# Optimization experiments

Measured on AMD Instinct MI355X. Metric: run time of the kernel, lower is better.

## Reference

```python
import jax, jax.numpy as jnp
import numpy as np

N_HEADS = 8
WINDOW = 4

def setup_inputs() -> dict:
    key = jax.random.key(0)
    ks = jax.random.split(key, 12)
    B, C, L = 8, 512, 1024
    Dh = C // N_HEADS
    s = 1.0 / np.sqrt(C)
    inp = {
        'x': jax.random.normal(ks[0], (B, C, L), dtype=jnp.float32),
        'Wq': jax.random.normal(ks[1], (C, C), dtype=jnp.float32) * s,
        'bq': jnp.zeros((C,), dtype=jnp.float32),
        'Wk': jax.random.normal(ks[2], (C, C), dtype=jnp.float32) * s,
        'bk': jnp.zeros((C,), dtype=jnp.float32),
        'Wv': jax.random.normal(ks[3], (C, C), dtype=jnp.float32) * s,
        'bv': jnp.zeros((C,), dtype=jnp.float32),
        'Wo': jax.random.normal(ks[4], (C, C), dtype=jnp.float32) * s,
        'bo': jnp.zeros((C,), dtype=jnp.float32),
        'emb_rel_k': jax.random.normal(ks[5], (2 * WINDOW + 1, Dh), dtype=jnp.float32) * 0.02,
        'emb_rel_v': jax.random.normal(ks[6], (2 * WINDOW + 1, Dh), dtype=jnp.float32) * 0.02,
    }
    return inp


def reference(x, Wq, bq, Wk, bk, Wv, bv, Wo, bo, emb_rel_k, emb_rel_v):
    B, C, L = x.shape
    H = N_HEADS
    Dh = C // H
    scale = Dh ** -0.5

    def proj(W, b):
        # pointwise conv1d == channel-mixing matmul; (B,C,L) -> (B,H,L,Dh)
        y = jnp.einsum('oc,bcl->bol', W, x) + b[:, None]
        return y.reshape(B, H, Dh, L).transpose(0, 1, 3, 2)

    q = proj(Wq, bq) * scale
    k = proj(Wk, bk)
    v = proj(Wv, bv)

    scores = jnp.einsum('bhld,bhjd->bhlj', q, k)  # (B,H,L,L)

    t = jnp.arange(L)
    diff = t[None, :] - t[:, None]                      # (L,L)
    window_mask = (jnp.abs(diff) <= WINDOW)
    indices = jnp.clip(diff, -WINDOW, WINDOW) + WINDOW  # (L,L) in [0, 2w]

    rel_k = emb_rel_k[indices]                          # (L,L,Dh)
    rel_scores = jnp.einsum('bhld,ljd->bhlj', q, rel_k)
    scores = scores + rel_scores * window_mask[None, None, :, :]

    attn = jax.nn.softmax(scores, axis=-1)

    out = jnp.einsum('bhlj,bhjd->bhld', attn, v)
    rel_v = emb_rel_v[indices] * window_mask[:, :, None]  # (L,L,Dh)
    out = out + jnp.einsum('bhlj,ljd->bhld', attn, rel_v)

    out = out.transpose(0, 1, 3, 2).reshape(B, C, L)
    out = jnp.einsum('oc,bcl->bol', Wo, out) + bo[:, None]
    return out
```

## Files before the change

kernel.cpp:

```cpp
#include <hip/hip_runtime.h>
#include <math.h>

#define B_  8
#define H_  8
#define C_  512
#define L_  1024
#define DH  64
#define WIN 4

typedef __attribute__((ext_vector_type(8))) short short8;
typedef __attribute__((ext_vector_type(4))) float floatx4;

__device__ __forceinline__ unsigned short f2bf(float f) {
    unsigned int u = __float_as_uint(f);
    u = u + 0x7FFFu + ((u >> 16) & 1u);
    return (unsigned short)(u >> 16);
}
__device__ __forceinline__ float bf2f(unsigned short h) {
    return __uint_as_float(((unsigned int)h) << 16);
}
__device__ __forceinline__ unsigned short f2h(float f) {
    _Float16 h = (_Float16)f;
    return *reinterpret_cast<unsigned short*>(&h);
}

__global__ __launch_bounds__(256) void prep_kernel(
    const float* __restrict__ Wq, const float* __restrict__ Wk,
    const float* __restrict__ Wv, const float* __restrict__ Wo,
    const float* __restrict__ bq, const float* __restrict__ bk,
    const float* __restrict__ bv,
    unsigned short* __restrict__ Wqkv_hi,
    unsigned short* __restrict__ Wo_h,
    float* __restrict__ bqkv)
{
    const int i = blockIdx.x * 256 + threadIdx.x;
    float4 v; ushort4 h;

    v = ((const float4*)Wq)[i];
    h.x = f2bf(v.x); h.y = f2bf(v.y); h.z = f2bf(v.z); h.w = f2bf(v.w);
    ((ushort4*)Wqkv_hi)[i] = h;

    v = ((const float4*)Wk)[i];
    h.x = f2bf(v.x); h.y = f2bf(v.y); h.z = f2bf(v.z); h.w = f2bf(v.w);
    ((ushort4*)Wqkv_hi)[65536 + i] = h;

    v = ((const float4*)Wv)[i];
    h.x = f2bf(v.x); h.y = f2bf(v.y); h.z = f2bf(v.z); h.w = f2bf(v.w);
    ((ushort4*)Wqkv_hi)[131072 + i] = h;

    v = ((const float4*)Wo)[i];
    h.x = f2h(v.x); h.y = f2h(v.y); h.z = f2h(v.z); h.w = f2h(v.w);
    ((ushort4*)Wo_h)[i] = h;

    if (i < 512)       bqkv[i] = bq[i];
    else if (i < 1024) bqkv[i] = bk[i - 512];
    else if (i < 1536) bqkv[i] = bv[i - 1024];
}

__global__ __launch_bounds__(256) void transpose_kernel(
    const float* __restrict__ x, unsigned short* __restrict__ xT)
{
    __shared__ float tile[32][33];
    const int b  = blockIdx.z;
    const int cb = blockIdx.y * 32;
    const int lb = blockIdx.x * 32;
    const int t  = threadIdx.x;
    {
        const int l = t & 31, c0 = t >> 5;
#pragma unroll
        for (int p = 0; p < 4; ++p) {
            const int c = c0 + 8 * p;
            tile[c][l] = x[((size_t)b * C_ + cb + c) * L_ + lb + l];
        }
    }
    __syncthreads();
    {
        const int c = t & 31, l0 = t >> 5;
#pragma unroll
        for (int p = 0; p < 4; ++p) {
            const int l = l0 + 8 * p;
            xT[((size_t)b * L_ + lb + l) * C_ + cb + c] = f2bf(tile[c][l]);
        }
    }
}

__global__ __launch_bounds__(256) void qkv_gemm_kernel(
    const unsigned short* __restrict__ Wh, const float* __restrict__ bqkv,
    const unsigned short* __restrict__ xT,
    unsigned short* __restrict__ Qb, unsigned short* __restrict__ Kb,
    unsigned short* __restrict__ Vc)
{
    __shared__ __align__(16) unsigned short As[128][40];
    __shared__ __align__(16) unsigned short Bs[128][40];
    __shared__ __align__(16) unsigned short sT[128][66];

    const int b   = blockIdx.z;
    const int oB  = blockIdx.y * 128;
    const int mat = oB >> 9;
    const int ob  = oB & 511;
    const int lb  = blockIdx.x * 128;
    const int t  = threadIdx.x;
    const int w = t >> 6, lane = t & 63, quad = lane >> 4, lc = lane & 15;
    const int wm = w >> 1, wn = w & 1;

    const unsigned short* Wm = Wh + (size_t)mat * C_ * C_;

    floatx4 acc[4][4];
#pragma unroll
    for (int i = 0; i < 4; ++i)
#pragma unroll
        for (int j = 0; j < 4; ++j) acc[i][j] = (floatx4)0.f;

    const int c8 = (t & 3) * 8, r0 = t >> 2;
    for (int c0 = 0; c0 < C_; c0 += 32) {
#pragma unroll
        for (int p = 0; p < 2; ++p) {
            *reinterpret_cast<uint4*>(&As[r0 + 64 * p][c8]) =
                *reinterpret_cast<const uint4*>(&Wm[(size_t)(ob + r0 + 64 * p) * C_ + c0 + c8]);
            *reinterpret_cast<uint4*>(&Bs[r0 + 64 * p][c8]) =
                *reinterpret_cast<const uint4*>(&xT[((size_t)b * L_ + lb + r0 + 64 * p) * C_ + c0 + c8]);
        }
        __syncthreads();

        short8 a[4], bb[4];
#pragma unroll
        for (int mt = 0; mt < 4; ++mt)
            a[mt] = *reinterpret_cast<const short8*>(&As[wm * 64 + mt * 16 + lc][quad * 8]);
#pragma unroll
        for (int nt = 0; nt < 4; ++nt)
            bb[nt] = *reinterpret_cast<const short8*>(&Bs[wn * 64 + nt * 16 + lc][quad * 8]);
#pragma unroll
        for (int mt = 0; mt < 4; ++mt)
#pragma unroll
            for (int nt = 0; nt < 4; ++nt)
                acc[mt][nt] = __builtin_amdgcn_mfma_f32_16x16x32_bf16(a[mt], bb[nt], acc[mt][nt], 0, 0, 0);
        __syncthreads();
    }

    if (mat == 2) {
#pragma unroll
        for (int mt = 0; mt < 4; ++mt) {
#pragma unroll
            for (int r = 0; r < 4; ++r) {
                const int o  = ob + wm * 64 + mt * 16 + quad * 4 + r;
                const float bi = bqkv[1024 + o];
#pragma unroll
                for (int nt = 0; nt < 4; ++nt) {
                    const int l = lb + wn * 64 + nt * 16 + lc;
                    Vc[((size_t)b * C_ + o) * L_ + l] = f2bf(acc[mt][nt][r] + bi);
                }
            }
        }
    } else {
        const float scale = (mat == 0) ? 0.125f : 1.0f;
        unsigned short* dst = (mat == 0) ? Qb : Kb;
#pragma unroll
        for (int hh = 0; hh < 2; ++hh) {
            if (wm == hh) {
#pragma unroll
                for (int mt = 0; mt < 4; ++mt) {
#pragma unroll
                    for (int r = 0; r < 4; ++r) {
                        const int o  = ob + hh * 64 + mt * 16 + quad * 4 + r;
                        const float bi = bqkv[mat * 512 + o];
                        const int d  = mt * 16 + quad * 4 + r;
#pragma unroll
                        for (int nt = 0; nt < 4; ++nt) {
                            const int l = wn * 64 + nt * 16 + lc;
                            sT[l][d] = f2bf((acc[mt][nt][r] + bi) * scale);
                        }
                    }
                }
            }
            __syncthreads();
            {
                const int l  = t >> 1, hf = t & 1;
                const int h  = (ob >> 6) + hh;
                const size_t o = (((size_t)b * H_ + h) * L_ + lb + l) * DH + hf * 32;
                uint4 v0 = *reinterpret_cast<const uint4*>(&sT[l][hf * 32]);
                uint4 v1 = *reinterpret_cast<const uint4*>(&sT[l][hf * 32 + 8]);
                uint4 v2 = *reinterpret_cast<const uint4*>(&sT[l][hf * 32 + 16]);
                uint4 v3 = *reinterpret_cast<const uint4*>(&sT[l][hf * 32 + 24]);
                *reinterpret_cast<uint4*>(&dst[o])      = v0;
                *reinterpret_cast<uint4*>(&dst[o + 8])  = v1;
                *reinterpret_cast<uint4*>(&dst[o + 16]) = v2;
                *reinterpret_cast<uint4*>(&dst[o + 24]) = v3;
            }
            __syncthreads();
        }
    }
}

__global__ __launch_bounds__(512, 4) void attn_kernel8(
    const unsigned short* __restrict__ Qb,
    const unsigned short* __restrict__ Kb,
    const unsigned short* __restrict__ Vc,
    const float* __restrict__ erel_k, const float* __restrict__ erel_v,
    unsigned short* __restrict__ AOh)
{
    __shared__ __align__(16) unsigned short kst[2][64][68];
    __shared__ __align__(16) unsigned short vst[2][64][68];
    __shared__ __align__(16) unsigned short Pl[8][16][68];
    __shared__ float rs[128][9];
    __shared__ float rv[128][9];

    const int t  = threadIdx.x;
    const int bh = blockIdx.x;
    const int rt = blockIdx.y;
    const int b = bh >> 3, h = bh & 7;
    const int w = t >> 6, lane = t & 63, quad = lane >> 4, lc = lane & 15;
    const int row0 = rt * 128;
    const int rowW = row0 + w * 16;

    const size_t qkBase = (size_t)bh * L_ * DH;
    const size_t vBase  = ((size_t)b * C_ + h * DH) * L_;

    for (int i = lane; i < 16 * 9; i += 64) rv[w * 16 + i / 9][i % 9] = 0.f;

    short8 af[2];
#pragma unroll
    for (int kk = 0; kk < 2; ++kk)
        af[kk] = *reinterpret_cast<const short8*>(
            &Qb[qkBase + (size_t)(rowW + lc) * DH + kk * 32 + quad * 8]);

    {
        floatx4 rsa = (floatx4)0.f;
        const int drow = (lc < 9) ? lc : 8;
#pragma unroll
        for (int kk = 0; kk < 2; ++kk) {
            short8 bfr;
#pragma unroll
            for (int i = 0; i < 8; ++i)
                bfr[i] = (short)f2bf(erel_k[drow * 64 + kk * 32 + quad * 8 + i]);
            rsa = __builtin_amdgcn_mfma_f32_16x16x32_bf16(af[kk], bfr, rsa, 0, 0, 0);
        }
        if (lc < 9) {
#pragma unroll
            for (int r = 0; r < 4; ++r)
                rs[w * 16 + quad * 4 + r][lc] = rsa[r];
        }
    }

    const int jr = t >> 3, jc = (t & 7) * 8;
    *reinterpret_cast<uint4*>(&kst[0][jr][jc]) =
        *reinterpret_cast<const uint4*>(&Kb[qkBase + (size_t)jr * DH + jc]);
    *reinterpret_cast<uint4*>(&vst[0][jr][jc]) =
        *reinterpret_cast<const uint4*>(&Vc[vBase + (size_t)jr * L_ + jc]);
    __syncthreads();

    short8 ones;
#pragma unroll
    for (int j = 0; j < 8; ++j) ones[j] = (short)0x3F80;

    floatx4 acc_o[4], acc_l = (floatx4)0.f;
#pragma unroll
    for (int nt = 0; nt < 4; ++nt) acc_o[nt] = (floatx4)0.f;

    for (int jt = 0; jt < L_ / 64; ++jt) {
        const int j0  = jt * 64;
        const int cur = jt & 1;

        uint4 pk, pv;
        if (jt < L_ / 64 - 1) {
            const int j0n = j0 + 64;
            pk = *reinterpret_cast<const uint4*>(
                &Kb[qkBase + (size_t)(j0n + jr) * DH + jc]);
            pv = *reinterpret_cast<const uint4*>(
                &Vc[vBase + (size_t)jr * L_ + j0n + jc]);
        }

        floatx4 sacc[4];
#pragma unroll
        for (int nt = 0; nt < 4; ++nt) sacc[nt] = (floatx4)0.f;
#pragma unroll
        for (int nt = 0; nt < 4; ++nt)
#pragma unroll
            for (int kk = 0; kk < 2; ++kk) {
                const short8 kf = *reinterpret_cast<const short8*>(
                    &kst[cur][nt * 16 + lc][kk * 32 + quad * 8]);
                sacc[nt] = __builtin_amdgcn_mfma_f32_16x16x32_bf16(af[kk], kf, sacc[nt], 0, 0, 0);
            }

        const bool nearD = (j0 <= rowW + 15 + WIN) && (j0 + 63 >= rowW - WIN);
        if (nearD) {
#pragma unroll
            for (int nt = 0; nt < 4; ++nt) {
                const int jg = j0 + nt * 16 + lc;
#pragma unroll
                for (int r = 0; r < 4; ++r) {
                    const int diff = jg - (rowW + quad * 4 + r);
                    if (diff >= -WIN && diff <= WIN)
                        sacc[nt][r] += rs[w * 16 + quad * 4 + r][diff + WIN];
                }
            }
        }

#pragma unroll
        for (int nt = 0; nt < 4; ++nt)
#pragma unroll
            for (int r = 0; r < 4; ++r)
                Pl[w][quad * 4 + r][nt * 16 + lc] = f2bf(__expf(sacc[nt][r]));

        if (nearD) {
            for (int idx = lane; idx < 16 * 9; idx += 64) {
                const int r16 = idx / 9, dr = idx % 9;
                const int jg = rowW + r16 + dr - WIN;
                if (jg >= j0 && jg < j0 + 64 && jg >= 0 && jg < L_)
                    rv[w * 16 + r16][dr] += bf2f(Pl[w][r16][jg - j0]);
            }
        }

        short8 pf[2];
#pragma unroll
        for (int kk = 0; kk < 2; ++kk)
            pf[kk] = *reinterpret_cast<const short8*>(&Pl[w][lc][kk * 32 + quad * 8]);

#pragma unroll
        for (int kk = 0; kk < 2; ++kk)
            acc_l = __builtin_amdgcn_mfma_f32_16x16x32_bf16(pf[kk], ones, acc_l, 0, 0, 0);

#pragma unroll
        for (int nt = 0; nt < 4; ++nt)
#pragma unroll
            for (int kk = 0; kk < 2; ++kk) {
                const short8 vf = *reinterpret_cast<const short8*>(
                    &vst[cur][nt * 16 + lc][kk * 32 + quad * 8]);
                acc_o[nt] = __builtin_amdgcn_mfma_f32_16x16x32_bf16(pf[kk], vf, acc_o[nt], 0, 0, 0);
            }

        if (jt < L_ / 64 - 1) {
            *reinterpret_cast<uint4*>(&kst[1 - cur][jr][jc]) = pk;
            *reinterpret_cast<uint4*>(&vst[1 - cur][jr][jc]) = pv;
        }
        __syncthreads();
    }

#pragma unroll
    for (int nt = 0; nt < 4; ++nt) {
        const int d = nt * 16 + lc;
        float ev[9];
#pragma unroll
        for (int dr = 0; dr < 9; ++dr) ev[dr] = erel_v[dr * 64 + d];
#pragma unroll
        for (int r = 0; r < 4; ++r) {
            const int rloc = w * 16 + quad * 4 + r;
            float v = acc_o[nt][r];
#pragma unroll
            for (int dr = 0; dr < 9; ++dr) v += rv[rloc][dr] * ev[dr];
            Pl[w][quad * 4 + r][nt * 16 + lc] = f2h(v / acc_l[r]);
        }
    }
    {
        const int row = lane >> 2, ds8 = (lane & 3) * 16;
        const uint4 q0 = *reinterpret_cast<const uint4*>(&Pl[w][row][ds8]);
        const uint4 q1 = *reinterpret_cast<const uint4*>(&Pl[w][row][ds8 + 8]);
        const size_t o = ((size_t)b * L_ + rowW + row) * C_ + h * 64 + ds8;
        *reinterpret_cast<uint4*>(&AOh[o])     = q0;
        *reinterpret_cast<uint4*>(&AOh[o + 8]) = q1;
    }
}

__global__ __launch_bounds__(256) void out_gemm_kernel(
    const unsigned short* __restrict__ Wh,
    const float* __restrict__ bo,
    const unsigned short* __restrict__ Ah,
    float* __restrict__ Y)
{
    __shared__ __align__(16) unsigned short As_h[128][40];
    __shared__ __align__(16) unsigned short Bs_h[64][40];

    const int b  = blockIdx.z;
    const int ob = blockIdx.y * 128;
    const int lb = blockIdx.x * 64;
    const int t  = threadIdx.x;
    const int w = t >> 6, lane = t & 63, quad = lane >> 4, lc = lane & 15;
    const int wm = w >> 1, wn = w & 1;

    floatx4 acc[4][2];
#pragma unroll
    for (int i = 0; i < 4; ++i)
#pragma unroll
        for (int j = 0; j < 2; ++j) acc[i][j] = (floatx4)0.f;

    const int c8 = (t & 3) * 8, r0 = t >> 2;
    for (int c0 = 0; c0 < C_; c0 += 32) {
#pragma unroll
        for (int p = 0; p < 2; ++p)
            *reinterpret_cast<uint4*>(&As_h[r0 + 64 * p][c8]) =
                *reinterpret_cast<const uint4*>(&Wh[(size_t)(ob + r0 + 64 * p) * C_ + c0 + c8]);
        {
            const size_t g = ((size_t)b * L_ + lb + r0) * C_ + c0 + c8;
            *reinterpret_cast<uint4*>(&Bs_h[r0][c8]) =
                *reinterpret_cast<const uint4*>(&Ah[g]);
        }
        __syncthreads();

        short8 ah[4], bhf[2];
#pragma unroll
        for (int mt = 0; mt < 4; ++mt)
            ah[mt] = *reinterpret_cast<const short8*>(&As_h[wm * 64 + mt * 16 + lc][quad * 8]);
#pragma unroll
        for (int nt = 0; nt < 2; ++nt)
            bhf[nt] = *reinterpret_cast<const short8*>(&Bs_h[wn * 32 + nt * 16 + lc][quad * 8]);
#pragma unroll
        for (int mt = 0; mt < 4; ++mt)
#pragma unroll
            for (int nt = 0; nt < 2; ++nt)
                acc[mt][nt] = __builtin_amdgcn_mfma_f32_16x16x32_f16(ah[mt], bhf[nt], acc[mt][nt], 0, 0, 0);
        __syncthreads();
    }

#pragma unroll
    for (int mt = 0; mt < 4; ++mt) {
#pragma unroll
        for (int r = 0; r < 4; ++r) {
            const int o = ob + wm * 64 + mt * 16 + quad * 4 + r;
            const float bi = bo[o];
#pragma unroll
            for (int nt = 0; nt < 2; ++nt) {
                const int l = lb + wn * 32 + nt * 16 + lc;
                Y[((size_t)b * C_ + o) * L_ + l] = acc[mt][nt][r] + bi;
            }
        }
    }
}

extern "C" void kernel_launch(void* const* d_in, const int* in_sizes, int n_in,
                              void* d_out, int out_size, void* d_ws, size_t ws_size,
                              hipStream_t stream)
{
    const float* x   = (const float*)d_in[0];
    const float* Wq  = (const float*)d_in[1];
    const float* bq  = (const float*)d_in[2];
    const float* Wk  = (const float*)d_in[3];
    const float* bk  = (const float*)d_in[4];
    const float* Wv  = (const float*)d_in[5];
    const float* bv  = (const float*)d_in[6];
    const float* Wo  = (const float*)d_in[7];
    const float* bo  = (const float*)d_in[8];
    const float* erk = (const float*)d_in[9];
    const float* erv = (const float*)d_in[10];

    char* ws = (char*)d_ws;
    const size_t MB = 1024u * 1024u;
    unsigned short* xT      = (unsigned short*)(ws);
    unsigned short* Qb      = (unsigned short*)(ws + 8 * MB);
    unsigned short* Kb      = (unsigned short*)(ws + 16 * MB);
    unsigned short* Vc      = (unsigned short*)(ws + 24 * MB);
    unsigned short* AOh     = (unsigned short*)(ws + 32 * MB);
    unsigned short* Wqkv_hi = (unsigned short*)(ws + 40 * MB);
    unsigned short* Wo_h    = (unsigned short*)(ws + 42 * MB);
    float*          bqkv    = (float*)(ws + 43 * MB);

    prep_kernel<<<256, 256, 0, stream>>>(Wq, Wk, Wv, Wo, bq, bk, bv,
                                         Wqkv_hi, Wo_h, bqkv);
    transpose_kernel<<<dim3(L_ / 32, C_ / 32, B_), 256, 0, stream>>>(x, xT);
    qkv_gemm_kernel<<<dim3(L_ / 128, 12, B_), 256, 0, stream>>>(
        Wqkv_hi, bqkv, xT, Qb, Kb, Vc);
    attn_kernel8<<<dim3(64, 8), 512, 0, stream>>>(
        Qb, Kb, Vc, erk, erv, AOh);
    out_gemm_kernel<<<dim3(L_ / 64, C_ / 128, B_), 256, 0, stream>>>(
        Wo_h, bo, AOh, (float*)d_out);
}
```

Measured before the change: 187.8 us.

## Double-buffer LDS tiles with register prefetch in QKV and output GEMMs

```diff
diff --git a/kernel.cpp b/kernel.cpp
--- a/kernel.cpp
+++ b/kernel.cpp
@@ -90,9 +90,7 @@
     unsigned short* __restrict__ Qb, unsigned short* __restrict__ Kb,
     unsigned short* __restrict__ Vc)
 {
-    __shared__ __align__(16) unsigned short As[128][40];
-    __shared__ __align__(16) unsigned short Bs[128][40];
-    __shared__ __align__(16) unsigned short sT[128][66];
+    __shared__ __align__(16) unsigned short AB[2][2][128][40];
 
     const int b   = blockIdx.z;
     const int oB  = blockIdx.y * 128;
@@ -112,28 +110,54 @@
         for (int j = 0; j < 4; ++j) acc[i][j] = (floatx4)0.f;
 
     const int c8 = (t & 3) * 8, r0 = t >> 2;
-    for (int c0 = 0; c0 < C_; c0 += 32) {
-#pragma unroll
-        for (int p = 0; p < 2; ++p) {
-            *reinterpret_cast<uint4*>(&As[r0 + 64 * p][c8]) =
-                *reinterpret_cast<const uint4*>(&Wm[(size_t)(ob + r0 + 64 * p) * C_ + c0 + c8]);
-            *reinterpret_cast<uint4*>(&Bs[r0 + 64 * p][c8]) =
-                *reinterpret_cast<const uint4*>(&xT[((size_t)b * L_ + lb + r0 + 64 * p) * C_ + c0 + c8]);
-        }
-        __syncthreads();
+
+#pragma unroll
+    for (int p = 0; p < 2; ++p) {
+        *reinterpret_cast<uint4*>(&AB[0][0][r0 + 64 * p][c8]) =
+            *reinterpret_cast<const uint4*>(&Wm[(size_t)(ob + r0 + 64 * p) * C_ + c8]);
+        *reinterpret_cast<uint4*>(&AB[1][0][r0 + 64 * p][c8]) =
+            *reinterpret_cast<const uint4*>(&xT[((size_t)b * L_ + lb + r0 + 64 * p) * C_ + c8]);
+    }
+    __syncthreads();
+
+    for (int s = 0; s < 16; ++s) {
+        const int cur = s & 1;
+
+        uint4 pa[2], pb[2];
+        if (s < 15) {
+            const int c0n = (s + 1) * 32;
+#pragma unroll
+            for (int p = 0; p < 2; ++p) {
+                pa[p] = *reinterpret_cast<const uint4*>(
+                    &Wm[(size_t)(ob + r0 + 64 * p) * C_ + c0n + c8]);
+                pb[p] = *reinterpret_cast<const uint4*>(
+                    &xT[((size_t)b * L_ + lb + r0 + 64 * p) * C_ + c0n + c8]);
+            }
+        }
 
         short8 a[4], bb[4];
 #pragma unroll
         for (int mt = 0; mt < 4; ++mt)
-            a[mt] = *reinterpret_cast<const short8*>(&As[wm * 64 + mt * 16 + lc][quad * 8]);
+            a[mt] = *reinterpret_cast<const short8*>(
+                &AB[0][cur][wm * 64 + mt * 16 + lc][quad * 8]);
 #pragma unroll
         for (int nt = 0; nt < 4; ++nt)
-            bb[nt] = *reinterpret_cast<const short8*>(&Bs[wn * 64 + nt * 16 + lc][quad * 8]);
+            bb[nt] = *reinterpret_cast<const short8*>(
+                &AB[1][cur][wn * 64 + nt * 16 + lc][quad * 8]);
 #pragma unroll
         for (int mt = 0; mt < 4; ++mt)
 #pragma unroll
             for (int nt = 0; nt < 4; ++nt)
-                acc[mt][nt] = __builtin_amdgcn_mfma_f32_16x16x32_bf16(a[mt], bb[nt], acc[mt][nt], 0, 0, 0);
+                acc[mt][nt] = __builtin_amdgcn_mfma_f32_16x16x32_bf16(
+                    a[mt], bb[nt], acc[mt][nt], 0, 0, 0);
+
+        if (s < 15) {
+#pragma unroll
+            for (int p = 0; p < 2; ++p) {
+                *reinterpret_cast<uint4*>(&AB[0][1 - cur][r0 + 64 * p][c8]) = pa[p];
+                *reinterpret_cast<uint4*>(&AB[1][1 - cur][r0 + 64 * p][c8]) = pb[p];
+            }
+        }
         __syncthreads();
     }
 
@@ -154,39 +178,40 @@
     } else {
         const float scale = (mat == 0) ? 0.125f : 1.0f;
         unsigned short* dst = (mat == 0) ? Qb : Kb;
-#pragma unroll
-        for (int hh = 0; hh < 2; ++hh) {
-            if (wm == hh) {
-#pragma unroll
-                for (int mt = 0; mt < 4; ++mt) {
-#pragma unroll
-                    for (int r = 0; r < 4; ++r) {
-                        const int o  = ob + hh * 64 + mt * 16 + quad * 4 + r;
-                        const float bi = bqkv[mat * 512 + o];
-                        const int d  = mt * 16 + quad * 4 + r;
-#pragma unroll
-                        for (int nt = 0; nt < 4; ++nt) {
-                            const int l = wn * 64 + nt * 16 + lc;
-                            sT[l][d] = f2bf((acc[mt][nt][r] + bi) * scale);
-                        }
-                    }
+        unsigned short (*sT)[144] =
+            reinterpret_cast<unsigned short (*)[144]>(&AB[0][0][0][0]);
+
+#pragma unroll
+        for (int mt = 0; mt < 4; ++mt) {
+#pragma unroll
+            for (int r = 0; r < 4; ++r) {
+                const int o  = ob + wm * 64 + mt * 16 + quad * 4 + r;
+                const float bi = bqkv[mat * 512 + o];
+                const int d  = mt * 16 + quad * 4 + r;
+#pragma unroll
+                for (int nt = 0; nt < 4; ++nt) {
+                    const int l = wn * 64 + nt * 16 + lc;
+                    sT[l][wm * 72 + d] = f2bf((acc[mt][nt][r] + bi) * scale);
                 }
             }
-            __syncthreads();
-            {
-                const int l  = t >> 1, hf = t & 1;
-                const int h  = (ob >> 6) + hh;
-                const size_t o = (((size_t)b * H_ + h) * L_ + lb + l) * DH + hf * 32;
-                uint4 v0 = *reinterpret_cast<const uint4*>(&sT[l][hf * 32]);
-                uint4 v1 = *reinterpret_cast<const uint4*>(&sT[l][hf * 32 + 8]);
-                uint4 v2 = *reinterpret_cast<const uint4*>(&sT[l][hf * 32 + 16]);
-                uint4 v3 = *reinterpret_cast<const uint4*>(&sT[l][hf * 32 + 24]);
+        }
+        __syncthreads();
+        {
+            const int l = t >> 1, hf = t & 1;
+#pragma unroll
+            for (int h01 = 0; h01 < 2; ++h01) {
+                const int hgl = (ob >> 6) + h01;
+                const size_t o = (((size_t)b * H_ + hgl) * L_ + lb + l) * DH + hf * 32;
+                const int cbase = h01 * 72 + hf * 32;
+                uint4 v0 = *reinterpret_cast<const uint4*>(&sT[l][cbase]);
+                uint4 v1 = *reinterpret_cast<const uint4*>(&sT[l][cbase + 8]);
+                uint4 v2 = *reinterpret_cast<const uint4*>(&sT[l][cbase + 16]);
+                uint4 v3 = *reinterpret_cast<const uint4*>(&sT[l][cbase + 24]);
                 *reinterpret_cast<uint4*>(&dst[o])      = v0;
                 *reinterpret_cast<uint4*>(&dst[o + 8])  = v1;
                 *reinterpret_cast<uint4*>(&dst[o + 16]) = v2;
                 *reinterpret_cast<uint4*>(&dst[o + 24]) = v3;
             }
-            __syncthreads();
         }
     }
 }
@@ -366,8 +391,8 @@
     const unsigned short* __restrict__ Ah,
     float* __restrict__ Y)
 {
-    __shared__ __align__(16) unsigned short As_h[128][40];
-    __shared__ __align__(16) unsigned short Bs_h[64][40];
+    __shared__ __align__(16) unsigned short Asb[2][128][40];
+    __shared__ __align__(16) unsigned short Bsb[2][64][40];
 
     const int b  = blockIdx.z;
     const int ob = blockIdx.y * 128;
@@ -383,30 +408,51 @@
         for (int j = 0; j < 2; ++j) acc[i][j] = (floatx4)0.f;
 
     const int c8 = (t & 3) * 8, r0 = t >> 2;
-    for (int c0 = 0; c0 < C_; c0 += 32) {
-#pragma unroll
-        for (int p = 0; p < 2; ++p)
-            *reinterpret_cast<uint4*>(&As_h[r0 + 64 * p][c8]) =
-                *reinterpret_cast<const uint4*>(&Wh[(size_t)(ob + r0 + 64 * p) * C_ + c0 + c8]);
-        {
-            const size_t g = ((size_t)b * L_ + lb + r0) * C_ + c0 + c8;
-            *reinterpret_cast<uint4*>(&Bs_h[r0][c8]) =
-                *reinterpret_cast<const uint4*>(&Ah[g]);
-        }
-        __syncthreads();
+
+#pragma unroll
+    for (int p = 0; p < 2; ++p)
+        *reinterpret_cast<uint4*>(&Asb[0][r0 + 64 * p][c8]) =
+            *reinterpret_cast<const uint4*>(&Wh[(size_t)(ob + r0 + 64 * p) * C_ + c8]);
+    *reinterpret_cast<uint4*>(&Bsb[0][r0][c8]) =
+        *reinterpret_cast<const uint4*>(&Ah[((size_t)b * L_ + lb + r0) * C_ + c8]);
+    __syncthreads();
+
+    for (int s = 0; s < 16; ++s) {
+        const int cur = s & 1;
+
+        uint4 pa[2], pb;
+        if (s < 15) {
+            const int c0n = (s + 1) * 32;
+#pragma unroll
+            for (int p = 0; p < 2; ++p)
+                pa[p] = *reinterpret_cast<const uint4*>(
+                    &Wh[(size_t)(ob + r0 + 64 * p) * C_ + c0n + c8]);
+            pb = *reinterpret_cast<const uint4*>(
+                &Ah[((size_t)b * L_ + lb + r0) * C_ + c0n + c8]);
+        }
 
         short8 ah[4], bhf[2];
 #pragma unroll
         for (int mt = 0; mt < 4; ++mt)
-            ah[mt] = *reinterpret_cast<const short8*>(&As_h[wm * 64 + mt * 16 + lc][quad * 8]);
+            ah[mt] = *reinterpret_cast<const short8*>(
+                &Asb[cur][wm * 64 + mt * 16 + lc][quad * 8]);
 #pragma unroll
         for (int nt = 0; nt < 2; ++nt)
-            bhf[nt] = *reinterpret_cast<const short8*>(&Bs_h[wn * 32 + nt * 16 + lc][quad * 8]);
+            bhf[nt] = *reinterpret_cast<const short8*>(
+                &Bsb[cur][wn * 32 + nt * 16 + lc][quad * 8]);
 #pragma unroll
         for (int mt = 0; mt < 4; ++mt)
 #pragma unroll
             for (int nt = 0; nt < 2; ++nt)
-                acc[mt][nt] = __builtin_amdgcn_mfma_f32_16x16x32_f16(ah[mt], bhf[nt], acc[mt][nt], 0, 0, 0);
+                acc[mt][nt] = __builtin_amdgcn_mfma_f32_16x16x32_f16(
+                    ah[mt], bhf[nt], acc[mt][nt], 0, 0, 0);
+
+        if (s < 15) {
+#pragma unroll
+            for (int p = 0; p < 2; ++p)
+                *reinterpret_cast<uint4*>(&Asb[1 - cur][r0 + 64 * p][c8]) = pa[p];
+            *reinterpret_cast<uint4*>(&Bsb[1 - cur][r0][c8]) = pb;
+        }
         __syncthreads();
     }
 
```

Result: faster. 173.4 us (-7.7%).
